# Optimization experiments

Measured on AMD Instinct MI355X. Metric: run time of the kernel, lower is better.

Reference implementation:

```python
import jax, jax.numpy as jnp
import numpy as np

N_HEADS = 16
D_MODEL = 1024
HEAD_DIM = D_MODEL // N_HEADS
B, S = 2, 2048


def setup_inputs() -> dict:
    key = jax.random.key(0)
    ks = jax.random.split(key, 10)
    scale = 1.0 / np.sqrt(D_MODEL)
    inp = {
        "query_tokens": jax.random.normal(ks[0], (B, S, D_MODEL), dtype=jnp.float32),
        "key_or_value_tokens": jax.random.normal(ks[1], (B, S, D_MODEL), dtype=jnp.float32),
        "mask": jnp.ones((B, S, S), dtype=jnp.int32),
        "Wq": jax.random.normal(ks[2], (D_MODEL, D_MODEL), dtype=jnp.float32) * scale,
        "bq": jnp.zeros((D_MODEL,), dtype=jnp.float32),
        "Wk": jax.random.normal(ks[3], (D_MODEL, D_MODEL), dtype=jnp.float32) * scale,
        "bk": jnp.zeros((D_MODEL,), dtype=jnp.float32),
        "Wv": jax.random.normal(ks[4], (D_MODEL, D_MODEL), dtype=jnp.float32) * scale,
        "bv": jnp.zeros((D_MODEL,), dtype=jnp.float32),
        "Wo": jax.random.normal(ks[5], (D_MODEL, D_MODEL), dtype=jnp.float32) * scale,
        "bo": jnp.zeros((D_MODEL,), dtype=jnp.float32),
    }
    return inp


def reference(query_tokens, key_or_value_tokens, mask, Wq, bq, Wk, bk, Wv, bv, Wo, bo):
    b, s, d = query_tokens.shape
    h, dh = N_HEADS, HEAD_DIM

    def proj(x, W, bias):
        # torch Linear: x @ W.T + b ; then split heads -> (b, h, s, dh)
        y = jnp.einsum("bsd,ed->bse", x, W) + bias
        return y.reshape(b, -1, h, dh).transpose(0, 2, 1, 3)

    q = proj(query_tokens, Wq, bq)
    k = proj(key_or_value_tokens, Wk, bk)
    v = proj(key_or_value_tokens, Wv, bv)

    scores = jnp.einsum("bhqd,bhkd->bhqk", q, k) / jnp.sqrt(jnp.float32(dh))
    # mask: (b, Sq, Sk) -> (b, 1, Sq, Sk); zeros get large negative fill
    scores = jnp.where(mask[:, None, :, :] == 0, jnp.float32(-1e9), scores)
    attn = jax.nn.softmax(scores, axis=-1)
    out = jnp.einsum("bhqk,bhkd->bhqd", attn, v)
    out = out.transpose(0, 2, 1, 3).reshape(b, s, d)
    return jnp.einsum("bsd,ed->bse", out, Wo) + bo
```

## Files before the change

kernel.cpp:

```cpp
#include <hip/hip_runtime.h>
#include <hip/hip_bf16.h>

typedef __bf16 bf16_8  __attribute__((ext_vector_type(8)));
typedef __bf16 bf16_4  __attribute__((ext_vector_type(4)));
typedef float  f32_4   __attribute__((ext_vector_type(4)));

#define NH 16
#define DHD 64
#define BB 2
#define SS 2048
#define DD 1024

__device__ __forceinline__ void gload16(const __bf16* g, __bf16* l) {
    __builtin_amdgcn_global_load_lds(
        (const __attribute__((address_space(1))) void*)g,
        (__attribute__((address_space(3))) void*)l, 16, 0, 0);
}

__global__ __launch_bounds__(256) void conv_all(
    const float* __restrict__ s0, const float* __restrict__ s1,
    const float* __restrict__ s2, const float* __restrict__ s3,
    const float* __restrict__ s4, const float* __restrict__ s5,
    __bf16* __restrict__ d0, __bf16* __restrict__ d1, __bf16* __restrict__ d2,
    __bf16* __restrict__ d3, __bf16* __restrict__ d4, __bf16* __restrict__ d5) {
    const int y = blockIdx.y;
    if (y >= 2 && blockIdx.x >= 1024) return;
    const float* s = (y == 0) ? s0 : (y == 1) ? s1 : (y == 2) ? s2
                   : (y == 3) ? s3 : (y == 4) ? s4 : s5;
    __bf16* d      = (y == 0) ? d0 : (y == 1) ? d1 : (y == 2) ? d2
                   : (y == 3) ? d3 : (y == 4) ? d4 : d5;
    const int i = (blockIdx.x * 256 + threadIdx.x) * 4;
    f32_4 v = *(const f32_4*)&s[i];
    bf16_4 o; o[0] = (__bf16)v[0]; o[1] = (__bf16)v[1];
    o[2] = (__bf16)v[2]; o[3] = (__bf16)v[3];
    *(bf16_4*)&d[i] = o;
}

__global__ __launch_bounds__(256) void mask_flags_k(const int* __restrict__ mask,
                                                    int* __restrict__ flags) {
    const int id = blockIdx.x;
    const int b = id >> 10, qt = (id >> 5) & 31, kt = id & 31;
    const int t = threadIdx.x;
    const int row = t >> 2, seg = t & 3;
    const int* p = mask + ((size_t)b * SS + qt * 64 + row) * SS + kt * 64 + seg * 16;
    int any0 = 0;
#pragma unroll
    for (int i = 0; i < 4; ++i) {
        int4 v = *(const int4*)&p[i * 4];
        any0 |= (v.x == 0) | (v.y == 0) | (v.z == 0) | (v.w == 0);
    }
    unsigned long long bal = __ballot(any0);
    __shared__ int sf[4];
    if ((t & 63) == 0) sf[t >> 6] = (bal != 0ULL);
    __syncthreads();
    if (t == 0) flags[id] = sf[0] | sf[1] | sf[2] | sf[3];
}

template <int LAYOUT>
__device__ __forceinline__ void gemm_body(const __bf16* __restrict__ A,
                                          const __bf16* __restrict__ W,
                                          const float* __restrict__ bias,
                                          __bf16* __restrict__ out,
                                          __bf16* ldsA, __bf16* ldsB) {
    const int tid  = threadIdx.x;
    const int lane = tid & 63;
    const int w    = tid >> 6;
    const int quad = lane >> 4;
    const int l15  = lane & 15;
    const int wm   = (w >> 1) * 64;
    const int wn   = (w & 1) * 64;
    const int m0   = blockIdx.x * 128;
    const int n0   = blockIdx.y * 128;

    f32_4 acc[4][4] = {};

    for (int kt = 0; kt < 1024; kt += 32) {
#pragma unroll
        for (int cc = 0; cc < 2; ++cc) {
            const int c   = tid + cc * 256;
            const int row = c >> 2;
            const int cp  = c & 3;
            gload16(&A[(size_t)(m0 + row) * 1024 + kt + cp * 8], &ldsA[c * 8]);
            gload16(&W[(size_t)(n0 + row) * 1024 + kt + cp * 8], &ldsB[c * 8]);
        }
        __syncthreads();

        bf16_8 af[4], bfr[4];
#pragma unroll
        for (int i = 0; i < 4; ++i)
            af[i] = *(const bf16_8*)&ldsA[(wm + i * 16 + l15) * 32 + quad * 8];
#pragma unroll
        for (int j = 0; j < 4; ++j)
            bfr[j] = *(const bf16_8*)&ldsB[(wn + j * 16 + l15) * 32 + quad * 8];
#pragma unroll
        for (int i = 0; i < 4; ++i)
#pragma unroll
            for (int j = 0; j < 4; ++j)
                acc[i][j] = __builtin_amdgcn_mfma_f32_16x16x32_bf16(
                    af[i], bfr[j], acc[i][j], 0, 0, 0);
        __syncthreads();
    }

#pragma unroll
    for (int i = 0; i < 4; ++i) {
#pragma unroll
        for (int j = 0; j < 4; ++j) {
            const int col = n0 + wn + j * 16 + l15;
            const float bv = bias[col];
            if (LAYOUT == 2) {
                const int row0 = m0 + wm + i * 16 + quad * 4;
                bf16_4 pk;
#pragma unroll
                for (int r = 0; r < 4; ++r) pk[r] = (__bf16)(acc[i][j][r] + bv);
                const int bb = row0 >> 11, s0 = row0 & 2047;
                const int h = col >> 6, dh = col & 63;
                *(bf16_4*)&out[(((size_t)bb * NH + h) * DHD + dh) * SS + s0] = pk;
            } else {
#pragma unroll
                for (int r = 0; r < 4; ++r) {
                    const int row = m0 + wm + i * 16 + quad * 4 + r;
                    out[(((size_t)(row >> 11) * NH + (col >> 6)) * SS +
                         (row & 2047)) * DHD + (col & 63)] =
                        (__bf16)(acc[i][j][r] + bv);
                }
            }
        }
    }
}

__global__ __launch_bounds__(256) void gemm_qkv(
    const __bf16* __restrict__ Xq, const __bf16* __restrict__ Xkv,
    const __bf16* __restrict__ Wq, const float* __restrict__ bq,
    const __bf16* __restrict__ Wk, const float* __restrict__ bk,
    const __bf16* __restrict__ Wv, const float* __restrict__ bv,
    __bf16* __restrict__ Qo, __bf16* __restrict__ Ko, __bf16* __restrict__ VTo) {
    __shared__ __align__(16) __bf16 ldsA[128 * 32];
    __shared__ __align__(16) __bf16 ldsB[128 * 32];
    const int z = blockIdx.z;
    const __bf16* A    = (z == 0) ? Xq : Xkv;
    const __bf16* W    = (z == 0) ? Wq : (z == 1 ? Wk : Wv);
    const float* bias  = (z == 0) ? bq : (z == 1 ? bk : bv);
    if (z == 2)
        gemm_body<2>(A, W, bias, VTo, ldsA, ldsB);
    else
        gemm_body<0>(A, W, bias, (z == 0) ? Qo : Ko, ldsA, ldsB);
}

__global__ __launch_bounds__(256) void gemm_final(
    const __bf16* __restrict__ A, const __bf16* __restrict__ W,
    const float* __restrict__ bias, float* __restrict__ out) {
    __shared__ __align__(16) __bf16 ldsA[64 * 32];
    __shared__ __align__(16) __bf16 ldsB[64 * 32];
    const int tid  = threadIdx.x;
    const int lane = tid & 63;
    const int w    = tid >> 6;
    const int quad = lane >> 4;
    const int l15  = lane & 15;
    const int wm   = (w >> 1) * 32;
    const int wn   = (w & 1) * 32;
    const int m0   = blockIdx.x * 64;
    const int n0   = blockIdx.y * 64;

    const int isB = w >> 1;
    const __bf16* src = isB ? W : A;
    const int     bN  = isB ? n0 : m0;
    __bf16*       dst = isB ? ldsB : ldsA;
    const int     w2  = w & 1;

    f32_4 acc[2][2] = {};

    for (int kt = 0; kt < 1024; kt += 32) {
#pragma unroll
        for (int cc = 0; cc < 2; ++cc) {
            const int c   = w2 * 128 + cc * 64 + lane;
            const int row = c >> 2;
            const int cp  = c & 3;
            gload16(&src[(size_t)(bN + row) * 1024 + kt + cp * 8], &dst[c * 8]);
        }
        __syncthreads();

        bf16_8 af[2], bfr[2];
#pragma unroll
        for (int i = 0; i < 2; ++i)
            af[i] = *(const bf16_8*)&ldsA[(wm + i * 16 + l15) * 32 + quad * 8];
#pragma unroll
        for (int j = 0; j < 2; ++j)
            bfr[j] = *(const bf16_8*)&ldsB[(wn + j * 16 + l15) * 32 + quad * 8];
#pragma unroll
        for (int i = 0; i < 2; ++i)
#pragma unroll
            for (int j = 0; j < 2; ++j)
                acc[i][j] = __builtin_amdgcn_mfma_f32_16x16x32_bf16(
                    af[i], bfr[j], acc[i][j], 0, 0, 0);
        __syncthreads();
    }

#pragma unroll
    for (int i = 0; i < 2; ++i)
#pragma unroll
        for (int j = 0; j < 2; ++j) {
            const int col = n0 + wn + j * 16 + l15;
            const float bv = bias[col];
#pragma unroll
            for (int r = 0; r < 4; ++r) {
                const int row = m0 + wm + i * 16 + quad * 4 + r;
                out[(size_t)row * 1024 + col] = acc[i][j][r] + bv;
            }
        }
}

__global__ __launch_bounds__(256, 2) void flash_attn(
    const __bf16* __restrict__ Q, const __bf16* __restrict__ K,
    const __bf16* __restrict__ VT, const int* __restrict__ mask,
    const int* __restrict__ flags, __bf16* __restrict__ O) {
    __shared__ __align__(16) __bf16 ldsK[64 * 72];
    __shared__ __align__(16) __bf16 ldsVT[64 * 72];
    __shared__ __align__(16) __bf16 ldsP[128 * 72];

    const int tid  = threadIdx.x;
    const int lane = tid & 63;
    const int w    = tid >> 6;
    const int quad = lane >> 4;
    const int l15  = lane & 15;
    const int q0   = blockIdx.x * 128;
    const int bh   = blockIdx.y;
    const int b    = bh >> 4;

    const __bf16* Qb  = Q + (size_t)bh * SS * DHD;
    const __bf16* Kb  = K + (size_t)bh * SS * DHD;
    const __bf16* VTb = VT + (size_t)bh * DHD * SS;
    const int*    mb  = mask + (size_t)b * SS * SS;
    const int*    flb = flags + (size_t)b * 1024 + blockIdx.x * 64;

    bf16_8 qa[2][2];
#pragma unroll
    for (int mt = 0; mt < 2; ++mt)
#pragma unroll
        for (int ks = 0; ks < 2; ++ks) {
            bf16_8 t = *(const bf16_8*)&Qb[(size_t)(q0 + w * 32 + mt * 16 + l15) * DHD +
                                           ks * 32 + quad * 8];
#pragma unroll
            for (int e = 0; e < 8; ++e)
                qa[mt][ks][e] = (__bf16)((float)t[e] * 0.18033688011112042f);
        }

    f32_4 of[2][4] = {};
    float li[2][4] = {};

    const int r0 = tid >> 3;
    const int r1 = r0 + 32;
    const int cp = tid & 7;
    uint4 kr0 = *(const uint4*)&Kb[(size_t)r0 * DHD + cp * 8];
    uint4 kr1 = *(const uint4*)&Kb[(size_t)r1 * DHD + cp * 8];
    uint4 vr0 = *(const uint4*)&VTb[(size_t)r0 * SS + cp * 8];
    uint4 vr1 = *(const uint4*)&VTb[(size_t)r1 * SS + cp * 8];

    for (int k0 = 0; k0 < SS; k0 += 64) {
        *(uint4*)&ldsK[r0 * 72 + cp * 8]  = kr0;
        *(uint4*)&ldsK[r1 * 72 + cp * 8]  = kr1;
        *(uint4*)&ldsVT[r0 * 72 + cp * 8] = vr0;
        *(uint4*)&ldsVT[r1 * 72 + cp * 8] = vr1;
        if (k0 + 64 < SS) {
            const int kn = k0 + 64;
            kr0 = *(const uint4*)&Kb[(size_t)(kn + r0) * DHD + cp * 8];
            kr1 = *(const uint4*)&Kb[(size_t)(kn + r1) * DHD + cp * 8];
            vr0 = *(const uint4*)&VTb[(size_t)r0 * SS + kn + cp * 8];
            vr1 = *(const uint4*)&VTb[(size_t)r1 * SS + kn + cp * 8];
        }
        __syncthreads();

        const bool msk = ((flb[k0 >> 6] | flb[32 + (k0 >> 6)]) != 0);

        f32_4 sa[2][4] = {};
#pragma unroll
        for (int ks = 0; ks < 2; ++ks) {
            bf16_8 kb[4];
#pragma unroll
            for (int j = 0; j < 4; ++j)
                kb[j] = *(const bf16_8*)&ldsK[(j * 16 + l15) * 72 + ks * 32 + quad * 8];
#pragma unroll
            for (int mt = 0; mt < 2; ++mt)
#pragma unroll
                for (int j = 0; j < 4; ++j)
                    sa[mt][j] = __builtin_amdgcn_mfma_f32_16x16x32_bf16(
                        qa[mt][ks], kb[j], sa[mt][j], 0, 0, 0);
        }

        if (msk) {
#pragma unroll
            for (int mt = 0; mt < 2; ++mt)
#pragma unroll
                for (int j = 0; j < 4; ++j)
#pragma unroll
                    for (int r = 0; r < 4; ++r) {
                        const int qg = q0 + w * 32 + mt * 16 + quad * 4 + r;
                        const int kg = k0 + j * 16 + l15;
                        if (mb[(size_t)qg * SS + kg] == 0) sa[mt][j][r] = -1e9f;
                    }
        }

#pragma unroll
        for (int mt = 0; mt < 2; ++mt)
#pragma unroll
            for (int j = 0; j < 4; ++j)
#pragma unroll
                for (int r = 0; r < 4; ++r) {
                    const float p = exp2f(sa[mt][j][r]);
                    li[mt][r] += p;
                    ldsP[(w * 32 + mt * 16 + quad * 4 + r) * 72 + j * 16 + l15] =
                        (__bf16)p;
                }
        __syncthreads();

#pragma unroll
        for (int ks2 = 0; ks2 < 2; ++ks2) {
            bf16_8 pa[2], vb[4];
#pragma unroll
            for (int mt = 0; mt < 2; ++mt)
                pa[mt] = *(const bf16_8*)&ldsP[(w * 32 + mt * 16 + l15) * 72 +
                                               ks2 * 32 + quad * 8];
#pragma unroll
            for (int jo = 0; jo < 4; ++jo)
                vb[jo] = *(const bf16_8*)&ldsVT[(jo * 16 + l15) * 72 +
                                                ks2 * 32 + quad * 8];
#pragma unroll
            for (int mt = 0; mt < 2; ++mt)
#pragma unroll
                for (int jo = 0; jo < 4; ++jo)
                    of[mt][jo] = __builtin_amdgcn_mfma_f32_16x16x32_bf16(
                        pa[mt], vb[jo], of[mt][jo], 0, 0, 0);
        }
        __syncthreads();
    }

    const int hcol = (bh & 15) * 64;
#pragma unroll
    for (int mt = 0; mt < 2; ++mt)
#pragma unroll
        for (int r = 0; r < 4; ++r) {
            float ls = li[mt][r];
            ls += __shfl_xor(ls, 1);
            ls += __shfl_xor(ls, 2);
            ls += __shfl_xor(ls, 4);
            ls += __shfl_xor(ls, 8);
            const float inv = 1.0f / fmaxf(ls, 1e-37f);
            const int qg = q0 + w * 32 + mt * 16 + quad * 4 + r;
#pragma unroll
            for (int jo = 0; jo < 4; ++jo)
                O[((size_t)b * SS + qg) * DD + hcol + jo * 16 + l15] =
                    (__bf16)(of[mt][jo][r] * inv);
        }
}


extern "C" void kernel_launch(void* const* d_in, const int* in_sizes, int n_in,
                              void* d_out, int out_size, void* d_ws, size_t ws_size,
                              hipStream_t stream) {
    const float* xq   = (const float*)d_in[0];
    const float* xkv  = (const float*)d_in[1];
    const int*   mask = (const int*)d_in[2];
    const float* Wq   = (const float*)d_in[3];
    const float* bq   = (const float*)d_in[4];
    const float* Wk   = (const float*)d_in[5];
    const float* bk   = (const float*)d_in[6];
    const float* Wv   = (const float*)d_in[7];
    const float* bv   = (const float*)d_in[8];
    const float* Wo   = (const float*)d_in[9];
    const float* bo   = (const float*)d_in[10];

    __bf16* ws = (__bf16*)d_ws;
    const size_t big = (size_t)BB * SS * DD;
    const size_t wsz = (size_t)DD * DD;
    __bf16* Qw   = ws;
    __bf16* Kw   = Qw + big;
    __bf16* VTw  = Kw + big;
    __bf16* Aw   = VTw + big;
    __bf16* Xqb  = Aw + big;
    __bf16* Xkvb = Xqb + big;
    __bf16* Wqb  = Xkvb + big;
    __bf16* Wkb  = Wqb + wsz;
    __bf16* Wvb  = Wkb + wsz;
    __bf16* Wob  = Wvb + wsz;
    int* flags   = (int*)(Wob + wsz);

    conv_all<<<dim3(4096, 6), dim3(256), 0, stream>>>(xq, xkv, Wq, Wk, Wv, Wo,
                                                      Xqb, Xkvb, Wqb, Wkb, Wvb, Wob);
    mask_flags_k<<<dim3(2048), dim3(256), 0, stream>>>(mask, flags);
    gemm_qkv<<<dim3(32, 8, 3), dim3(256), 0, stream>>>(Xqb, Xkvb, Wqb, bq, Wkb, bk,
                                                       Wvb, bv, Qw, Kw, VTw);
    flash_attn<<<dim3(SS / 128, BB * NH), dim3(256), 0, stream>>>(Qw, Kw, VTw, mask,
                                                                  flags, Aw);
    gemm_final<<<dim3(64, 16), dim3(256), 0, stream>>>(Aw, Wob, bo, (float*)d_out);
}
```

Baseline: 268.1 us.

## Split flash attention over two key halves and combine partial sums

Result: slower. 280.2 us (+4.5%).

```diff
diff --git a/kernel.cpp b/kernel.cpp
--- a/kernel.cpp
+++ b/kernel.cpp
@@ -209,13 +209,15 @@
         }
 }
 
+#define PST 76
 __global__ __launch_bounds__(256, 2) void flash_attn(
     const __bf16* __restrict__ Q, const __bf16* __restrict__ K,
     const __bf16* __restrict__ VT, const int* __restrict__ mask,
-    const int* __restrict__ flags, __bf16* __restrict__ O) {
+    const int* __restrict__ flags, float* __restrict__ Opart,
+    float* __restrict__ lpart) {
     __shared__ __align__(16) __bf16 ldsK[64 * 72];
     __shared__ __align__(16) __bf16 ldsVT[64 * 72];
-    __shared__ __align__(16) __bf16 ldsP[128 * 72];
+    __shared__ __align__(16) __bf16 ldsP[128 * PST];
 
     const int tid  = threadIdx.x;
     const int lane = tid & 63;
@@ -225,12 +227,17 @@
     const int q0   = blockIdx.x * 128;
     const int bh   = blockIdx.y;
     const int b    = bh >> 4;
+    const int kz   = blockIdx.z;
+    const int kbeg = kz * (SS / 2);
+    const int kend = kbeg + (SS / 2);
 
     const __bf16* Qb  = Q + (size_t)bh * SS * DHD;
     const __bf16* Kb  = K + (size_t)bh * SS * DHD;
     const __bf16* VTb = VT + (size_t)bh * DHD * SS;
     const int*    mb  = mask + (size_t)b * SS * SS;
     const int*    flb = flags + (size_t)b * 1024 + blockIdx.x * 64;
+    float* Op = Opart + (size_t)kz * BB * SS * DD;
+    float* lp = lpart + (size_t)kz * BB * NH * SS;
 
     bf16_8 qa[2][2];
 #pragma unroll
@@ -250,17 +257,17 @@
     const int r0 = tid >> 3;
     const int r1 = r0 + 32;
     const int cp = tid & 7;
-    uint4 kr0 = *(const uint4*)&Kb[(size_t)r0 * DHD + cp * 8];
-    uint4 kr1 = *(const uint4*)&Kb[(size_t)r1 * DHD + cp * 8];
-    uint4 vr0 = *(const uint4*)&VTb[(size_t)r0 * SS + cp * 8];
-    uint4 vr1 = *(const uint4*)&VTb[(size_t)r1 * SS + cp * 8];
-
-    for (int k0 = 0; k0 < SS; k0 += 64) {
+    uint4 kr0 = *(const uint4*)&Kb[(size_t)(kbeg + r0) * DHD + cp * 8];
+    uint4 kr1 = *(const uint4*)&Kb[(size_t)(kbeg + r1) * DHD + cp * 8];
+    uint4 vr0 = *(const uint4*)&VTb[(size_t)r0 * SS + kbeg + cp * 8];
+    uint4 vr1 = *(const uint4*)&VTb[(size_t)r1 * SS + kbeg + cp * 8];
+
+    for (int k0 = kbeg; k0 < kend; k0 += 64) {
         *(uint4*)&ldsK[r0 * 72 + cp * 8]  = kr0;
         *(uint4*)&ldsK[r1 * 72 + cp * 8]  = kr1;
         *(uint4*)&ldsVT[r0 * 72 + cp * 8] = vr0;
         *(uint4*)&ldsVT[r1 * 72 + cp * 8] = vr1;
-        if (k0 + 64 < SS) {
+        if (k0 + 64 < kend) {
             const int kn = k0 + 64;
             kr0 = *(const uint4*)&Kb[(size_t)(kn + r0) * DHD + cp * 8];
             kr1 = *(const uint4*)&Kb[(size_t)(kn + r1) * DHD + cp * 8];
@@ -307,7 +314,7 @@
                 for (int r = 0; r < 4; ++r) {
                     const float p = exp2f(sa[mt][j][r]);
                     li[mt][r] += p;
-                    ldsP[(w * 32 + mt * 16 + quad * 4 + r) * 72 + j * 16 + l15] =
+                    ldsP[(w * 32 + mt * 16 + quad * 4 + r) * PST + j * 16 + l15] =
                         (__bf16)p;
                 }
         __syncthreads();
@@ -317,7 +324,7 @@
             bf16_8 pa[2], vb[4];
 #pragma unroll
             for (int mt = 0; mt < 2; ++mt)
-                pa[mt] = *(const bf16_8*)&ldsP[(w * 32 + mt * 16 + l15) * 72 +
+                pa[mt] = *(const bf16_8*)&ldsP[(w * 32 + mt * 16 + l15) * PST +
                                                ks2 * 32 + quad * 8];
 #pragma unroll
             for (int jo = 0; jo < 4; ++jo)
@@ -343,13 +350,31 @@
             ls += __shfl_xor(ls, 2);
             ls += __shfl_xor(ls, 4);
             ls += __shfl_xor(ls, 8);
-            const float inv = 1.0f / fmaxf(ls, 1e-37f);
             const int qg = q0 + w * 32 + mt * 16 + quad * 4 + r;
+            if (l15 == 0) lp[(size_t)bh * SS + qg] = ls;
 #pragma unroll
             for (int jo = 0; jo < 4; ++jo)
-                O[((size_t)b * SS + qg) * DD + hcol + jo * 16 + l15] =
-                    (__bf16)(of[mt][jo][r] * inv);
-        }
+                Op[((size_t)b * SS + qg) * DD + hcol + jo * 16 + l15] = of[mt][jo][r];
+        }
+}
+
+__global__ __launch_bounds__(256) void combine(
+    const float* __restrict__ Opart, const float* __restrict__ lpart,
+    __bf16* __restrict__ out) {
+    const int idx = (blockIdx.x * 256 + threadIdx.x) * 4;
+    const int d = idx & (DD - 1);
+    const int s = (idx >> 10) & (SS - 1);
+    const int b = idx >> 21;
+    const int bh = b * NH + (d >> 6);
+    const float l = lpart[(size_t)bh * SS + s] +
+                    lpart[(size_t)BB * NH * SS + (size_t)bh * SS + s];
+    const float inv = 1.0f / fmaxf(l, 1e-37f);
+    f32_4 a = *(const f32_4*)&Opart[idx];
+    f32_4 c = *(const f32_4*)&Opart[(size_t)BB * SS * DD + idx];
+    bf16_4 o;
+#pragma unroll
+    for (int e = 0; e < 4; ++e) o[e] = (__bf16)((a[e] + c[e]) * inv);
+    *(bf16_4*)&out[idx] = o;
 }
 
 
@@ -382,13 +407,20 @@
     __bf16* Wvb  = Wkb + wsz;
     __bf16* Wob  = Wvb + wsz;
     int* flags   = (int*)(Wob + wsz);
+    float* Opart0 = (float*)Xqb;
+    float* Opart1 = (float*)(flags + 2048);
+    float* lpart0 = Opart1 + big;
+    float* OpartC = (float*)(flags + 2048);
+    float* lpartC = OpartC + 2 * big;
+    (void)Opart0; (void)Opart1; (void)lpart0;
 
     conv_all<<<dim3(4096, 6), dim3(256), 0, stream>>>(xq, xkv, Wq, Wk, Wv, Wo,
                                                       Xqb, Xkvb, Wqb, Wkb, Wvb, Wob);
     mask_flags_k<<<dim3(2048), dim3(256), 0, stream>>>(mask, flags);
     gemm_qkv<<<dim3(32, 8, 3), dim3(256), 0, stream>>>(Xqb, Xkvb, Wqb, bq, Wkb, bk,
                                                        Wvb, bv, Qw, Kw, VTw);
-    flash_attn<<<dim3(SS / 128, BB * NH), dim3(256), 0, stream>>>(Qw, Kw, VTw, mask,
-                                                                  flags, Aw);
+    flash_attn<<<dim3(SS / 128, BB * NH, 2), dim3(256), 0, stream>>>(
+        Qw, Kw, VTw, mask, flags, OpartC, lpartC);
+    combine<<<dim3(4096), dim3(256), 0, stream>>>(OpartC, lpartC, Aw);
     gemm_final<<<dim3(64, 16), dim3(256), 0, stream>>>(Aw, Wob, bo, (float*)d_out);
 }
```
